# Performance work log

Measured on AMD Instinct MI355X. Metric: run time of the kernel, lower is better.

Reference implementation:

```python
import jax, jax.numpy as jnp
import numpy as np


def _maxpool2x2(t):
    # t: [B, C, H, W] -> [B, C, H//2, W//2]
    B, C, H, W = t.shape
    return t.reshape(B, C, H // 2, 2, W // 2, 2).max(axis=(3, 5))


def setup_inputs() -> dict:
    key = jax.random.key(0)
    k_x, k_t, k_p, k_g, k_o = jax.random.split(key, 5)
    B, C, H, W = 16, 256, 64, 64
    C8, C2 = C // 8, C // 2
    scale = 1.0 / np.sqrt(C)
    return {
        "x": jax.random.normal(k_x, (B, C, H, W), dtype=jnp.float32),
        "w_theta": jax.random.normal(k_t, (C8, C), dtype=jnp.float32) * scale,
        "w_phi": jax.random.normal(k_p, (C8, C), dtype=jnp.float32) * scale,
        "w_g": jax.random.normal(k_g, (C2, C), dtype=jnp.float32) * scale,
        "w_o": jax.random.normal(k_o, (C, C2), dtype=jnp.float32) * (1.0 / np.sqrt(C2)),
        "gamma": jnp.ones((), dtype=jnp.float32),
    }


def reference(x, w_theta, w_phi, w_g, w_o, gamma):
    B, C, H, W = x.shape
    C8, C2 = C // 8, C // 2
    HW = H * W
    # 1x1 conv projections (pure channel GEMMs)
    theta = jnp.einsum("oc,bchw->bohw", w_theta, x)            # [B, C8, H, W]
    phi = _maxpool2x2(jnp.einsum("oc,bchw->bohw", w_phi, x))   # [B, C8, H/2, W/2]
    g = _maxpool2x2(jnp.einsum("oc,bchw->bohw", w_g, x))       # [B, C2, H/2, W/2]
    theta = theta.reshape(B, C8, HW)            # [B, C8, HW]
    phi = phi.reshape(B, C8, HW // 4)           # [B, C8, HW/4]
    g = g.reshape(B, C2, HW // 4)               # [B, C2, HW/4]
    # attention: no scaling, single head (BigGAN style)
    scores = jnp.einsum("bct,bcp->btp", theta, phi)   # [B, HW, HW/4]
    beta = jax.nn.softmax(scores, axis=-1)
    attn = jnp.einsum("bcp,btp->bct", g, beta)        # [B, C2, HW]
    attn = attn.reshape(B, C2, H, W)
    o = jnp.einsum("oc,bchw->bohw", w_o, attn)        # [B, C, H, W]
    return gamma * o + x
```

## Files before the change

### kernel.cpp

```cpp
#include <hip/hip_runtime.h>
#include <stdint.h>


#define B_  16
#define C_  256
#define HW_ 4096
#define C8_ 32
#define C2_ 128
#define P_  1024

#define WS_THETA 0u
#define WS_PHI   2097152u
#define WS_G     2621440u
#define WS_WOG   4718592u
#define WS_BETA  6815744u

__device__ inline unsigned short f2bf(float f) {
    unsigned int u = __builtin_bit_cast(unsigned int, f);
    u = (u + 0x7fffu + ((u >> 16) & 1u)) >> 16;
    return (unsigned short)u;
}
__device__ inline void beta_store4(unsigned short* p, float a, float b, float c, float d) {
    ushort4 v; v.x = f2bf(a); v.y = f2bf(b); v.z = f2bf(c); v.w = f2bf(d);
    *(ushort4*)p = v;
}
__device__ inline void splitbf(float f, unsigned short& h, unsigned short& l) {
    unsigned u = __builtin_bit_cast(unsigned, f);
    h = (unsigned short)(u >> 16);
    float lof = f - __builtin_bit_cast(float, u & 0xffff0000u);
    l = (unsigned short)(__builtin_bit_cast(unsigned, lof) >> 16);
}

typedef __attribute__((ext_vector_type(8))) short bf16x8;
typedef __attribute__((ext_vector_type(8))) unsigned short u16x8;
typedef __attribute__((ext_vector_type(4))) float f32x4;

#define GLOAD_LDS(gsrc, ldst) __builtin_amdgcn_global_load_lds( \
    (__attribute__((address_space(1))) void*)(uintptr_t)(const void*)(gsrc), \
    (__attribute__((address_space(3))) void*)(ldst), 16, 0, 0)

__global__ __launch_bounds__(256, 3) void k1_proj(
    const float* __restrict__ x, const float* __restrict__ w_theta,
    const float* __restrict__ w_phi, const float* __restrict__ w_g,
    float* __restrict__ thetaT_o, float* __restrict__ phiT_o, float* __restrict__ g_o)
{
    const int ht = blockIdx.x, ogrp = blockIdx.y, b = blockIdx.z;
    const int tid = threadIdx.x;
    const int lane = tid & 63, wv = tid >> 6;
    const int lr = lane & 15, lk = lane >> 4;

    __shared__ float xs[64 * 128];
    __shared__ unsigned short WHs[64 * 72];
    __shared__ unsigned short WLs[64 * 72];

    const float* xb = x + ((size_t)b * C_) * HW_ + (size_t)ht * 128;
    const int c_ld = tid >> 2;
    const int sseg = (tid & 3) * 32;
    const int o_ld = tid >> 2;
    const int cseg = (tid & 3) * 16;

    const float* wsrc;
    if (ogrp == 0) wsrc = (o_ld < 32) ? (w_theta + o_ld * 256)
                                      : (w_phi + (o_ld - 32) * 256);
    else if (ogrp == 1) wsrc = w_g + o_ld * 256;
    else wsrc = w_g + (o_ld + 64) * 256;

    f32x4 acc[4][2] = {};

    for (int kc = 0; kc < 4; ++kc) {
        const int c0 = kc * 64;
        __syncthreads();
        {
            const float* src = xb + (size_t)(c0 + c_ld) * HW_ + sseg;
            #pragma unroll
            for (int u = 0; u < 8; ++u)
                *(float4*)&xs[c_ld * 128 + sseg + u * 4] = *(const float4*)&src[u * 4];
        }
        {
            #pragma unroll
            for (int h = 0; h < 2; ++h) {
                u16x8 hi, lo;
                #pragma unroll
                for (int e = 0; e < 8; ++e) {
                    unsigned short hh, ll;
                    splitbf(wsrc[c0 + cseg + h * 8 + e], hh, ll);
                    hi[e] = hh; lo[e] = ll;
                }
                *(u16x8*)&WHs[o_ld * 72 + cseg + h * 8] = hi;
                *(u16x8*)&WLs[o_ld * 72 + cseg + h * 8] = lo;
            }
        }
        __syncthreads();

        #pragma unroll
        for (int ks = 0; ks < 2; ++ks) {
            bf16x8 Ah[4], Al[4];
            #pragma unroll
            for (int mf = 0; mf < 4; ++mf) {
                Ah[mf] = *(const bf16x8*)&WHs[(mf * 16 + lr) * 72 + ks * 32 + lk * 8];
                Al[mf] = *(const bf16x8*)&WLs[(mf * 16 + lr) * 72 + ks * 32 + lk * 8];
            }
            #pragma unroll
            for (int nf = 0; nf < 2; ++nf) {
                const int s = wv * 32 + nf * 16 + lr;
                u16x8 hi, lo;
                #pragma unroll
                for (int e = 0; e < 8; ++e) {
                    unsigned short hh, ll;
                    splitbf(xs[(ks * 32 + lk * 8 + e) * 128 + s], hh, ll);
                    hi[e] = hh; lo[e] = ll;
                }
                const bf16x8 Bh = __builtin_bit_cast(bf16x8, hi);
                const bf16x8 Bl = __builtin_bit_cast(bf16x8, lo);
                #pragma unroll
                for (int mf = 0; mf < 4; ++mf) {
                    acc[mf][nf] = __builtin_amdgcn_mfma_f32_16x16x32_bf16(
                        Ah[mf], Bh, acc[mf][nf], 0, 0, 0);
                    acc[mf][nf] = __builtin_amdgcn_mfma_f32_16x16x32_bf16(
                        Ah[mf], Bl, acc[mf][nf], 0, 0, 0);
                    acc[mf][nf] = __builtin_amdgcn_mfma_f32_16x16x32_bf16(
                        Al[mf], Bh, acc[mf][nf], 0, 0, 0);
                }
            }
        }
    }

    __syncthreads();
    #pragma unroll
    for (int mf = 0; mf < 4; ++mf)
        #pragma unroll
        for (int nf = 0; nf < 2; ++nf)
            #pragma unroll
            for (int r = 0; r < 4; ++r)
                xs[(mf * 16 + lk * 4 + r) * 128 + wv * 32 + nf * 16 + lr]
                    = acc[mf][nf][r];
    __syncthreads();

    if (ogrp == 0) {
        {
            const int s = tid >> 1, o16 = (tid & 1) * 16;
            float* dst = thetaT_o + ((size_t)b * HW_ + (size_t)ht * 128 + s) * 32 + o16;
            #pragma unroll
            for (int u = 0; u < 4; ++u) {
                float4 v;
                v.x = xs[(o16 + u * 4 + 0) * 128 + s];
                v.y = xs[(o16 + u * 4 + 1) * 128 + s];
                v.z = xs[(o16 + u * 4 + 2) * 128 + s];
                v.w = xs[(o16 + u * 4 + 3) * 128 + s];
                *(float4*)&dst[u * 4] = v;
            }
        }
        {
            const int o2 = tid >> 3, wq = (tid & 7) * 4;
            #pragma unroll
            for (int u = 0; u < 4; ++u) {
                int w2 = wq + u;
                float pv = fmaxf(fmaxf(xs[(32 + o2) * 128 + 2 * w2],
                                       xs[(32 + o2) * 128 + 2 * w2 + 1]),
                                 fmaxf(xs[(32 + o2) * 128 + 64 + 2 * w2],
                                       xs[(32 + o2) * 128 + 64 + 2 * w2 + 1]));
                phiT_o[((size_t)b * P_ + (size_t)ht * 32 + w2) * 32 + o2] = pv;
            }
        }
    } else {
        const int base = (ogrp - 1) * 64;
        const int o = tid >> 2, wq = (tid & 3) * 8;
        float* dst = g_o + ((size_t)b * C2_ + base + o) * P_ + (size_t)ht * 32 + wq;
        #pragma unroll
        for (int u = 0; u < 8; ++u) {
            int w2 = wq + u;
            dst[u] = fmaxf(fmaxf(xs[o * 128 + 2 * w2], xs[o * 128 + 2 * w2 + 1]),
                           fmaxf(xs[o * 128 + 64 + 2 * w2], xs[o * 128 + 64 + 2 * w2 + 1]));
        }
    }
}

__global__ __launch_bounds__(256) void k2_wog(
    const float* __restrict__ w_o, const float* __restrict__ g,
    unsigned short* __restrict__ wog)
{
    const int p0 = blockIdx.x * 64, cb = blockIdx.y, b = blockIdx.z;
    const int tid = threadIdx.x, wv = tid >> 6, lane = tid & 63;
    __shared__ float wls[64][128];
    __shared__ float gls[128][64];

    {
        const int o = tid >> 2, q = (tid & 3) * 32;
        const float* src = w_o + (size_t)(cb * 64 + o) * 128 + q;
        #pragma unroll
        for (int u = 0; u < 8; ++u)
            *(float4*)&wls[o][q + u * 4] = *(const float4*)&src[u * 4];
        const int c2 = tid >> 1, h = (tid & 1) * 32;
        const float* gsrc = g + ((size_t)b * C2_ + c2) * P_ + p0 + h;
        #pragma unroll
        for (int u = 0; u < 8; ++u)
            *(float4*)&gls[c2][h + u * 4] = *(const float4*)&gsrc[u * 4];
    }
    __syncthreads();

    float acc[16] = {};
    for (int k4 = 0; k4 < 32; ++k4) {
        float gk[4];
        #pragma unroll
        for (int kk = 0; kk < 4; ++kk) gk[kk] = gls[k4 * 4 + kk][lane];
        #pragma unroll
        for (int i = 0; i < 16; ++i) {
            float4 w4 = *(const float4*)&wls[wv * 16 + i][k4 * 4];
            acc[i] += w4.x * gk[0] + w4.y * gk[1] + w4.z * gk[2] + w4.w * gk[3];
        }
    }
    #pragma unroll
    for (int i = 0; i < 16; ++i)
        wog[((size_t)b * C_ + cb * 64 + wv * 16 + i) * P_ + p0 + lane] = f2bf(acc[i]);
}

__global__ __launch_bounds__(256, 3) void k3_mfma(
    const float* __restrict__ thetaT, const float* __restrict__ phiT,
    unsigned short* __restrict__ beta)
{
    const int t0 = blockIdx.x * 16, b = blockIdx.y;
    const int tid = threadIdx.x, wv = tid >> 6, lane = tid & 63;
    const int lr = lane & 15, lk = lane >> 4;

    __shared__ __align__(16) char sm[44032];
    unsigned short* phH = (unsigned short*)sm;
    unsigned short* phL = (unsigned short*)(sm + 20480);
    unsigned short* thH = (unsigned short*)(sm + 40960);
    unsigned short* thL = (unsigned short*)(sm + 42240);
    float* red = (float*)(sm + 43520);

    if (tid < 128) {
        const int t = tid >> 3, c4 = (tid & 7) * 4;
        float4 v = *(const float4*)&thetaT[((size_t)b * HW_ + t0 + t) * 32 + c4];
        ushort4 hv, lv;
        splitbf(v.x, hv.x, lv.x); splitbf(v.y, hv.y, lv.y);
        splitbf(v.z, hv.z, lv.z); splitbf(v.w, hv.w, lv.w);
        *(ushort4*)&thH[t * 40 + c4] = hv;
        *(ushort4*)&thL[t * 40 + c4] = lv;
    }

    f32x4 sc[16];

    #pragma unroll
    for (int ch = 0; ch < 4; ++ch) {
        __syncthreads();
        {
            const float* src = &phiT[((size_t)b * P_ + ch * 256 + tid) * 32];
            #pragma unroll
            for (int g2 = 0; g2 < 4; ++g2) {
                float4 a = *(const float4*)&src[g2 * 8];
                float4 b4 = *(const float4*)&src[g2 * 8 + 4];
                u16x8 hi, lo;
                unsigned short hh, ll;
                splitbf(a.x, hh, ll);  hi[0] = hh; lo[0] = ll;
                splitbf(a.y, hh, ll);  hi[1] = hh; lo[1] = ll;
                splitbf(a.z, hh, ll);  hi[2] = hh; lo[2] = ll;
                splitbf(a.w, hh, ll);  hi[3] = hh; lo[3] = ll;
                splitbf(b4.x, hh, ll); hi[4] = hh; lo[4] = ll;
                splitbf(b4.y, hh, ll); hi[5] = hh; lo[5] = ll;
                splitbf(b4.z, hh, ll); hi[6] = hh; lo[6] = ll;
                splitbf(b4.w, hh, ll); hi[7] = hh; lo[7] = ll;
                *(u16x8*)&phH[tid * 40 + g2 * 8] = hi;
                *(u16x8*)&phL[tid * 40 + g2 * 8] = lo;
            }
        }
        __syncthreads();

        const bf16x8 Ah = *(const bf16x8*)&thH[lr * 40 + lk * 8];
        const bf16x8 Al = *(const bf16x8*)&thL[lr * 40 + lk * 8];
        #pragma unroll
        for (int q = 0; q < 4; ++q) {
            const int prow = wv * 64 + q * 16 + lr;
            const bf16x8 Bh = *(const bf16x8*)&phH[prow * 40 + lk * 8];
            const bf16x8 Bl = *(const bf16x8*)&phL[prow * 40 + lk * 8];
            f32x4 a = {};
            a = __builtin_amdgcn_mfma_f32_16x16x32_bf16(Ah, Bh, a, 0, 0, 0);
            a = __builtin_amdgcn_mfma_f32_16x16x32_bf16(Ah, Bl, a, 0, 0, 0);
            a = __builtin_amdgcn_mfma_f32_16x16x32_bf16(Al, Bh, a, 0, 0, 0);
            sc[ch * 4 + q] = a;
        }
    }

    float mrow[4], rl[4];
    #pragma unroll
    for (int r = 0; r < 4; ++r) {
        float m = sc[0][r];
        #pragma unroll
        for (int qg = 1; qg < 16; ++qg) m = fmaxf(m, sc[qg][r]);
        #pragma unroll
        for (int off = 1; off < 16; off <<= 1) m = fmaxf(m, __shfl_xor(m, off));
        mrow[r] = m;
    }
    __syncthreads();
    if (lr == 0) {
        #pragma unroll
        for (int r = 0; r < 4; ++r) red[(lk * 4 + r) * 4 + wv] = mrow[r];
    }
    __syncthreads();
    #pragma unroll
    for (int r = 0; r < 4; ++r) {
        const int t = lk * 4 + r;
        mrow[r] = fmaxf(fmaxf(red[t * 4 + 0], red[t * 4 + 1]),
                        fmaxf(red[t * 4 + 2], red[t * 4 + 3]));
    }
    __syncthreads();

    float ssum[4];
    #pragma unroll
    for (int r = 0; r < 4; ++r) {
        float s = 0.f;
        #pragma unroll
        for (int qg = 0; qg < 16; ++qg) {
            float e = __expf(sc[qg][r] - mrow[r]);
            sc[qg][r] = e; s += e;
        }
        #pragma unroll
        for (int off = 1; off < 16; off <<= 1) s += __shfl_xor(s, off);
        ssum[r] = s;
    }
    if (lr == 0) {
        #pragma unroll
        for (int r = 0; r < 4; ++r) red[(lk * 4 + r) * 4 + wv] = ssum[r];
    }
    __syncthreads();
    #pragma unroll
    for (int r = 0; r < 4; ++r) {
        const int t = lk * 4 + r;
        rl[r] = 1.0f / (red[t * 4 + 0] + red[t * 4 + 1] +
                        red[t * 4 + 2] + red[t * 4 + 3]);
    }

    unsigned short* bb = beta + ((size_t)b * HW_ + t0) * P_;
    #pragma unroll
    for (int qg = 0; qg < 16; ++qg) {
        const int p = (qg >> 2) * 256 + wv * 64 + (qg & 3) * 16 + lr;
        #pragma unroll
        for (int r = 0; r < 4; ++r)
            bb[(size_t)(lk * 4 + r) * P_ + p] = f2bf(sc[qg][r] * rl[r]);
    }
}

__global__ __launch_bounds__(256) void k4_mfma(
    const unsigned short* __restrict__ wog, const unsigned short* __restrict__ beta,
    const float* __restrict__ x, const float* __restrict__ gamma_p,
    float* __restrict__ out)
{
    const int t0 = blockIdx.x * 128, c0 = blockIdx.y * 128, b = blockIdx.z;
    const int tid = threadIdx.x, wv = tid >> 6, lane = tid & 63;
    const int wm = wv >> 1, wn = wv & 1;
    const int lr = lane & 15, lk = lane >> 4;
    __shared__ unsigned short As[128 * 64];
    __shared__ unsigned short Bs[128 * 64];

    f32x4 acc[4][4] = {};
    const unsigned short* wog_b  = wog  + ((size_t)b * C_  + c0) * P_;
    const unsigned short* beta_b = beta + ((size_t)b * HW_ + t0) * P_;

    for (int p0 = 0; p0 < 1024; p0 += 64) {
        __syncthreads();
        #pragma unroll
        for (int ch = 0; ch < 4; ++ch) {
            const int i16 = ch * 256 + tid;
            const int row = i16 >> 3, cb8 = i16 & 7;
            GLOAD_LDS(wog_b  + (size_t)row * P_ + p0 + cb8 * 8, &As[i16 * 8]);
            GLOAD_LDS(beta_b + (size_t)row * P_ + p0 + cb8 * 8, &Bs[i16 * 8]);
        }
        __syncthreads();

        #pragma unroll
        for (int ks = 0; ks < 2; ++ks) {
            bf16x8 af[4], bfr[4];
            #pragma unroll
            for (int mf = 0; mf < 4; ++mf)
                af[mf] = *(const bf16x8*)&As[(wm * 64 + mf * 16 + lr) * 64 + ks * 32 + lk * 8];
            #pragma unroll
            for (int nf = 0; nf < 4; ++nf)
                bfr[nf] = *(const bf16x8*)&Bs[(wn * 64 + nf * 16 + lr) * 64 + ks * 32 + lk * 8];
            #pragma unroll
            for (int mf = 0; mf < 4; ++mf)
                #pragma unroll
                for (int nf = 0; nf < 4; ++nf)
                    acc[mf][nf] = __builtin_amdgcn_mfma_f32_16x16x32_bf16(
                        af[mf], bfr[nf], acc[mf][nf], 0, 0, 0);
        }
    }

    const float gm = gamma_p[0];
    #pragma unroll
    for (int mf = 0; mf < 4; ++mf) {
        #pragma unroll
        for (int r = 0; r < 4; ++r) {
            const int co = c0 + wm * 64 + mf * 16 + lk * 4 + r;
            const size_t rowoff = ((size_t)b * C_ + co) * HW_;
            #pragma unroll
            for (int nf = 0; nf < 4; ++nf) {
                const int t = t0 + wn * 64 + nf * 16 + lr;
                out[rowoff + t] = gm * acc[mf][nf][r] + x[rowoff + t];
            }
        }
    }
}

extern "C" void kernel_launch(void* const* d_in, const int* in_sizes, int n_in,
                              void* d_out, int out_size, void* d_ws, size_t ws_size,
                              hipStream_t stream)
{
    const float* x       = (const float*)d_in[0];
    const float* w_theta = (const float*)d_in[1];
    const float* w_phi   = (const float*)d_in[2];
    const float* w_g     = (const float*)d_in[3];
    const float* w_o     = (const float*)d_in[4];
    const float* gamma   = (const float*)d_in[5];
    float* out = (float*)d_out;
    float* ws  = (float*)d_ws;

    float* thetaT         = ws + WS_THETA;
    float* phiT           = ws + WS_PHI;
    float* g              = ws + WS_G;
    unsigned short* wog   = (unsigned short*)(ws + WS_WOG);
    unsigned short* beta  = (unsigned short*)(ws + WS_BETA);

    k1_proj<<<dim3(32, 3, 16), 256, 0, stream>>>(x, w_theta, w_phi, w_g,
                                                 thetaT, phiT, g);
    k2_wog<<<dim3(16, 4, 16), 256, 0, stream>>>(w_o, g, wog);
    k3_mfma<<<dim3(256, 16), 256, 0, stream>>>(thetaT, phiT, beta);
    k4_mfma<<<dim3(32, 2, 16), 256, 0, stream>>>(wog, beta, x, gamma, out);
}
```

Measured before the change: 321.0 us.

## Presplit theta/phi to bf16 hi/lo in projection and enlarge score tiles

The projection kernel now writes theta and phi already split into bf16 high/low halves, so the score kernel no longer converts fp32 per block. The score kernel loads those halves directly into LDS with global_load_lds using an XOR swizzle, and processes 32 query rows per block instead of 16. This halves the number of phi reloads and conversions. k4's LDS tiles also get an XOR swizzle to reduce bank conflicts. In exchange, the score kernel holds twice as many accumulator registers and its occupancy hint drops from 3 to 2.

```diff
diff --git a/kernel.cpp b/kernel.cpp
--- a/kernel.cpp
+++ b/kernel.cpp
@@ -9,20 +9,18 @@
 #define C2_ 128
 #define P_  1024
 
-#define WS_THETA 0u
-#define WS_PHI   2097152u
-#define WS_G     2621440u
-#define WS_WOG   4718592u
-#define WS_BETA  6815744u
+#define WS_THH  0u
+#define WS_THL  1048576u
+#define WS_PHH  2097152u
+#define WS_PHL  2359296u
+#define WS_G    2621440u
+#define WS_WOG  4718592u
+#define WS_BETA 6815744u
 
 __device__ inline unsigned short f2bf(float f) {
     unsigned int u = __builtin_bit_cast(unsigned int, f);
     u = (u + 0x7fffu + ((u >> 16) & 1u)) >> 16;
     return (unsigned short)u;
-}
-__device__ inline void beta_store4(unsigned short* p, float a, float b, float c, float d) {
-    ushort4 v; v.x = f2bf(a); v.y = f2bf(b); v.z = f2bf(c); v.w = f2bf(d);
-    *(ushort4*)p = v;
 }
 __device__ inline void splitbf(float f, unsigned short& h, unsigned short& l) {
     unsigned u = __builtin_bit_cast(unsigned, f);
@@ -42,7 +40,9 @@
 __global__ __launch_bounds__(256, 3) void k1_proj(
     const float* __restrict__ x, const float* __restrict__ w_theta,
     const float* __restrict__ w_phi, const float* __restrict__ w_g,
-    float* __restrict__ thetaT_o, float* __restrict__ phiT_o, float* __restrict__ g_o)
+    unsigned short* __restrict__ thetaTH, unsigned short* __restrict__ thetaTL,
+    unsigned short* __restrict__ phiTH, unsigned short* __restrict__ phiTL,
+    float* __restrict__ g_o)
 {
     const int ht = blockIdx.x, ogrp = blockIdx.y, b = blockIdx.z;
     const int tid = threadIdx.x;
@@ -139,16 +139,18 @@
     if (ogrp == 0) {
         {
             const int s = tid >> 1, o16 = (tid & 1) * 16;
-            float* dst = thetaT_o + ((size_t)b * HW_ + (size_t)ht * 128 + s) * 32 + o16;
-            #pragma unroll
-            for (int u = 0; u < 4; ++u) {
-                float4 v;
-                v.x = xs[(o16 + u * 4 + 0) * 128 + s];
-                v.y = xs[(o16 + u * 4 + 1) * 128 + s];
-                v.z = xs[(o16 + u * 4 + 2) * 128 + s];
-                v.w = xs[(o16 + u * 4 + 3) * 128 + s];
-                *(float4*)&dst[u * 4] = v;
-            }
+            u16x8 h0, h1, l0, l1;
+            #pragma unroll
+            for (int i = 0; i < 8; ++i) {
+                unsigned short hh, ll;
+                splitbf(xs[(o16 + i) * 128 + s], hh, ll);
+                h0[i] = hh; l0[i] = ll;
+                splitbf(xs[(o16 + 8 + i) * 128 + s], hh, ll);
+                h1[i] = hh; l1[i] = ll;
+            }
+            const size_t roff = ((size_t)b * HW_ + (size_t)ht * 128 + s) * 32 + o16;
+            *(u16x8*)&thetaTH[roff] = h0; *(u16x8*)&thetaTH[roff + 8] = h1;
+            *(u16x8*)&thetaTL[roff] = l0; *(u16x8*)&thetaTL[roff + 8] = l1;
         }
         {
             const int o2 = tid >> 3, wq = (tid & 7) * 4;
@@ -159,7 +161,10 @@
                                        xs[(32 + o2) * 128 + 2 * w2 + 1]),
                                  fmaxf(xs[(32 + o2) * 128 + 64 + 2 * w2],
                                        xs[(32 + o2) * 128 + 64 + 2 * w2 + 1]));
-                phiT_o[((size_t)b * P_ + (size_t)ht * 32 + w2) * 32 + o2] = pv;
+                unsigned short hh, ll;
+                splitbf(pv, hh, ll);
+                const size_t poff = ((size_t)b * P_ + (size_t)ht * 32 + w2) * 32 + o2;
+                phiTH[poff] = hh; phiTL[poff] = ll;
             }
         }
     } else {
@@ -214,130 +219,139 @@
         wog[((size_t)b * C_ + cb * 64 + wv * 16 + i) * P_ + p0 + lane] = f2bf(acc[i]);
 }
 
-__global__ __launch_bounds__(256, 3) void k3_mfma(
-    const float* __restrict__ thetaT, const float* __restrict__ phiT,
+__global__ __launch_bounds__(256, 2) void k3_mfma(
+    const unsigned short* __restrict__ thH_g, const unsigned short* __restrict__ thL_g,
+    const unsigned short* __restrict__ phH_g, const unsigned short* __restrict__ phL_g,
     unsigned short* __restrict__ beta)
 {
-    const int t0 = blockIdx.x * 16, b = blockIdx.y;
+    const int t0 = blockIdx.x * 32, b = blockIdx.y;
     const int tid = threadIdx.x, wv = tid >> 6, lane = tid & 63;
     const int lr = lane & 15, lk = lane >> 4;
 
-    __shared__ __align__(16) char sm[44032];
-    unsigned short* phH = (unsigned short*)sm;
-    unsigned short* phL = (unsigned short*)(sm + 20480);
-    unsigned short* thH = (unsigned short*)(sm + 40960);
-    unsigned short* thL = (unsigned short*)(sm + 42240);
-    float* red = (float*)(sm + 43520);
-
-    if (tid < 128) {
-        const int t = tid >> 3, c4 = (tid & 7) * 4;
-        float4 v = *(const float4*)&thetaT[((size_t)b * HW_ + t0 + t) * 32 + c4];
-        ushort4 hv, lv;
-        splitbf(v.x, hv.x, lv.x); splitbf(v.y, hv.y, lv.y);
-        splitbf(v.z, hv.z, lv.z); splitbf(v.w, hv.w, lv.w);
-        *(ushort4*)&thH[t * 40 + c4] = hv;
-        *(ushort4*)&thL[t * 40 + c4] = lv;
-    }
-
-    f32x4 sc[16];
+    __shared__ unsigned short thH[32 * 32], thL[32 * 32];
+    __shared__ unsigned short phH[256 * 32], phL[256 * 32];
+    __shared__ float red[32 * 4];
+
+    {
+        const int u = lane + (wv & 1) * 64;
+        const int row = u >> 2, j = u & 3;
+        const int gj = j ^ ((row >> 1) & 3);
+        const size_t goff = ((size_t)b * HW_ + t0 + row) * 32 + gj * 8;
+        if (wv < 2) GLOAD_LDS(thH_g + goff, &thH[u * 8]);
+        else        GLOAD_LDS(thL_g + goff, &thL[u * 8]);
+    }
+
+    f32x4 sc[2][16] = {};
 
     #pragma unroll
     for (int ch = 0; ch < 4; ++ch) {
         __syncthreads();
-        {
-            const float* src = &phiT[((size_t)b * P_ + ch * 256 + tid) * 32];
-            #pragma unroll
-            for (int g2 = 0; g2 < 4; ++g2) {
-                float4 a = *(const float4*)&src[g2 * 8];
-                float4 b4 = *(const float4*)&src[g2 * 8 + 4];
-                u16x8 hi, lo;
-                unsigned short hh, ll;
-                splitbf(a.x, hh, ll);  hi[0] = hh; lo[0] = ll;
-                splitbf(a.y, hh, ll);  hi[1] = hh; lo[1] = ll;
-                splitbf(a.z, hh, ll);  hi[2] = hh; lo[2] = ll;
-                splitbf(a.w, hh, ll);  hi[3] = hh; lo[3] = ll;
-                splitbf(b4.x, hh, ll); hi[4] = hh; lo[4] = ll;
-                splitbf(b4.y, hh, ll); hi[5] = hh; lo[5] = ll;
-                splitbf(b4.z, hh, ll); hi[6] = hh; lo[6] = ll;
-                splitbf(b4.w, hh, ll); hi[7] = hh; lo[7] = ll;
-                *(u16x8*)&phH[tid * 40 + g2 * 8] = hi;
-                *(u16x8*)&phL[tid * 40 + g2 * 8] = lo;
-            }
-        }
-        __syncthreads();
-
-        const bf16x8 Ah = *(const bf16x8*)&thH[lr * 40 + lk * 8];
-        const bf16x8 Al = *(const bf16x8*)&thL[lr * 40 + lk * 8];
+        #pragma unroll
+        for (int it = 0; it < 4; ++it) {
+            const int u = it * 256 + tid;
+            const int row = u >> 2, j = u & 3;
+            const int gj = j ^ ((row >> 1) & 3);
+            const size_t goff = ((size_t)b * P_ + ch * 256 + row) * 32 + gj * 8;
+            GLOAD_LDS(phH_g + goff, &phH[u * 8]);
+            GLOAD_LDS(phL_g + goff, &phL[u * 8]);
+        }
+        __syncthreads();
+
+        bf16x8 Ah[2], Al[2];
+        #pragma unroll
+        for (int mf = 0; mf < 2; ++mf) {
+            const int tr = mf * 16 + lr;
+            const int ja = lk ^ ((tr >> 1) & 3);
+            Ah[mf] = *(const bf16x8*)&thH[tr * 32 + ja * 8];
+            Al[mf] = *(const bf16x8*)&thL[tr * 32 + ja * 8];
+        }
         #pragma unroll
         for (int q = 0; q < 4; ++q) {
-            const int prow = wv * 64 + q * 16 + lr;
-            const bf16x8 Bh = *(const bf16x8*)&phH[prow * 40 + lk * 8];
-            const bf16x8 Bl = *(const bf16x8*)&phL[prow * 40 + lk * 8];
-            f32x4 a = {};
-            a = __builtin_amdgcn_mfma_f32_16x16x32_bf16(Ah, Bh, a, 0, 0, 0);
-            a = __builtin_amdgcn_mfma_f32_16x16x32_bf16(Ah, Bl, a, 0, 0, 0);
-            a = __builtin_amdgcn_mfma_f32_16x16x32_bf16(Al, Bh, a, 0, 0, 0);
-            sc[ch * 4 + q] = a;
-        }
-    }
-
-    float mrow[4], rl[4];
-    #pragma unroll
-    for (int r = 0; r < 4; ++r) {
-        float m = sc[0][r];
-        #pragma unroll
-        for (int qg = 1; qg < 16; ++qg) m = fmaxf(m, sc[qg][r]);
-        #pragma unroll
-        for (int off = 1; off < 16; off <<= 1) m = fmaxf(m, __shfl_xor(m, off));
-        mrow[r] = m;
-    }
-    __syncthreads();
-    if (lr == 0) {
-        #pragma unroll
-        for (int r = 0; r < 4; ++r) red[(lk * 4 + r) * 4 + wv] = mrow[r];
-    }
-    __syncthreads();
-    #pragma unroll
-    for (int r = 0; r < 4; ++r) {
-        const int t = lk * 4 + r;
-        mrow[r] = fmaxf(fmaxf(red[t * 4 + 0], red[t * 4 + 1]),
-                        fmaxf(red[t * 4 + 2], red[t * 4 + 3]));
-    }
-    __syncthreads();
-
-    float ssum[4];
-    #pragma unroll
-    for (int r = 0; r < 4; ++r) {
-        float s = 0.f;
+            const int pr = wv * 64 + q * 16 + lr;
+            const int jb = lk ^ ((pr >> 1) & 3);
+            const bf16x8 Bh = *(const bf16x8*)&phH[pr * 32 + jb * 8];
+            const bf16x8 Bl = *(const bf16x8*)&phL[pr * 32 + jb * 8];
+            #pragma unroll
+            for (int mf = 0; mf < 2; ++mf) {
+                f32x4 a = sc[mf][ch * 4 + q];
+                a = __builtin_amdgcn_mfma_f32_16x16x32_bf16(Ah[mf], Bh, a, 0, 0, 0);
+                a = __builtin_amdgcn_mfma_f32_16x16x32_bf16(Ah[mf], Bl, a, 0, 0, 0);
+                a = __builtin_amdgcn_mfma_f32_16x16x32_bf16(Al[mf], Bh, a, 0, 0, 0);
+                sc[mf][ch * 4 + q] = a;
+            }
+        }
+    }
+
+    float mrow[2][4];
+    #pragma unroll
+    for (int mf = 0; mf < 2; ++mf)
+        #pragma unroll
+        for (int r = 0; r < 4; ++r) {
+            float m = sc[mf][0][r];
+            #pragma unroll
+            for (int qg = 1; qg < 16; ++qg) m = fmaxf(m, sc[mf][qg][r]);
+            #pragma unroll
+            for (int off = 1; off < 16; off <<= 1) m = fmaxf(m, __shfl_xor(m, off));
+            mrow[mf][r] = m;
+        }
+    if (lr == 0)
+        #pragma unroll
+        for (int mf = 0; mf < 2; ++mf)
+            #pragma unroll
+            for (int r = 0; r < 4; ++r)
+                red[(mf * 16 + lk * 4 + r) * 4 + wv] = mrow[mf][r];
+    __syncthreads();
+    #pragma unroll
+    for (int mf = 0; mf < 2; ++mf)
+        #pragma unroll
+        for (int r = 0; r < 4; ++r) {
+            const int t = mf * 16 + lk * 4 + r;
+            mrow[mf][r] = fmaxf(fmaxf(red[t * 4 + 0], red[t * 4 + 1]),
+                                fmaxf(red[t * 4 + 2], red[t * 4 + 3]));
+        }
+    __syncthreads();
+
+    float rl[2][4];
+    #pragma unroll
+    for (int mf = 0; mf < 2; ++mf)
+        #pragma unroll
+        for (int r = 0; r < 4; ++r) {
+            float s = 0.f;
+            #pragma unroll
+            for (int qg = 0; qg < 16; ++qg) {
+                float e = __expf(sc[mf][qg][r] - mrow[mf][r]);
+                sc[mf][qg][r] = e; s += e;
+            }
+            #pragma unroll
+            for (int off = 1; off < 16; off <<= 1) s += __shfl_xor(s, off);
+            rl[mf][r] = s;
+        }
+    if (lr == 0)
+        #pragma unroll
+        for (int mf = 0; mf < 2; ++mf)
+            #pragma unroll
+            for (int r = 0; r < 4; ++r)
+                red[(mf * 16 + lk * 4 + r) * 4 + wv] = rl[mf][r];
+    __syncthreads();
+    #pragma unroll
+    for (int mf = 0; mf < 2; ++mf)
+        #pragma unroll
+        for (int r = 0; r < 4; ++r) {
+            const int t = mf * 16 + lk * 4 + r;
+            rl[mf][r] = 1.0f / (red[t * 4 + 0] + red[t * 4 + 1] +
+                                red[t * 4 + 2] + red[t * 4 + 3]);
+        }
+
+    unsigned short* bb = beta + ((size_t)b * HW_ + t0) * P_;
+    #pragma unroll
+    for (int mf = 0; mf < 2; ++mf)
         #pragma unroll
         for (int qg = 0; qg < 16; ++qg) {
-            float e = __expf(sc[qg][r] - mrow[r]);
-            sc[qg][r] = e; s += e;
-        }
-        #pragma unroll
-        for (int off = 1; off < 16; off <<= 1) s += __shfl_xor(s, off);
-        ssum[r] = s;
-    }
-    if (lr == 0) {
-        #pragma unroll
-        for (int r = 0; r < 4; ++r) red[(lk * 4 + r) * 4 + wv] = ssum[r];
-    }
-    __syncthreads();
-    #pragma unroll
-    for (int r = 0; r < 4; ++r) {
-        const int t = lk * 4 + r;
-        rl[r] = 1.0f / (red[t * 4 + 0] + red[t * 4 + 1] +
-                        red[t * 4 + 2] + red[t * 4 + 3]);
-    }
-
-    unsigned short* bb = beta + ((size_t)b * HW_ + t0) * P_;
-    #pragma unroll
-    for (int qg = 0; qg < 16; ++qg) {
-        const int p = (qg >> 2) * 256 + wv * 64 + (qg & 3) * 16 + lr;
-        #pragma unroll
-        for (int r = 0; r < 4; ++r)
-            bb[(size_t)(lk * 4 + r) * P_ + p] = f2bf(sc[qg][r] * rl[r]);
-    }
+            const int p = (qg >> 2) * 256 + wv * 64 + (qg & 3) * 16 + lr;
+            #pragma unroll
+            for (int r = 0; r < 4; ++r)
+                bb[(size_t)(mf * 16 + lk * 4 + r) * P_ + p] = f2bf(sc[mf][qg][r] * rl[mf][r]);
+        }
 }
 
 __global__ __launch_bounds__(256) void k4_mfma(
@@ -362,8 +376,9 @@
         for (int ch = 0; ch < 4; ++ch) {
             const int i16 = ch * 256 + tid;
             const int row = i16 >> 3, cb8 = i16 & 7;
-            GLOAD_LDS(wog_b  + (size_t)row * P_ + p0 + cb8 * 8, &As[i16 * 8]);
-            GLOAD_LDS(beta_b + (size_t)row * P_ + p0 + cb8 * 8, &Bs[i16 * 8]);
+            const int gcb = cb8 ^ (row & 7);
+            GLOAD_LDS(wog_b  + (size_t)row * P_ + p0 + gcb * 8, &As[i16 * 8]);
+            GLOAD_LDS(beta_b + (size_t)row * P_ + p0 + gcb * 8, &Bs[i16 * 8]);
         }
         __syncthreads();
 
@@ -371,11 +386,17 @@
         for (int ks = 0; ks < 2; ++ks) {
             bf16x8 af[4], bfr[4];
             #pragma unroll
-            for (int mf = 0; mf < 4; ++mf)
-                af[mf] = *(const bf16x8*)&As[(wm * 64 + mf * 16 + lr) * 64 + ks * 32 + lk * 8];
-            #pragma unroll
-            for (int nf = 0; nf < 4; ++nf)
-                bfr[nf] = *(const bf16x8*)&Bs[(wn * 64 + nf * 16 + lr) * 64 + ks * 32 + lk * 8];
+            for (int mf = 0; mf < 4; ++mf) {
+                const int arow = wm * 64 + mf * 16 + lr;
+                const int ja = (ks * 4 + lk) ^ (arow & 7);
+                af[mf] = *(const bf16x8*)&As[arow * 64 + ja * 8];
+            }
+            #pragma unroll
+            for (int nf = 0; nf < 4; ++nf) {
+                const int brow = wn * 64 + nf * 16 + lr;
+                const int jb = (ks * 4 + lk) ^ (brow & 7);
+                bfr[nf] = *(const bf16x8*)&Bs[brow * 64 + jb * 8];
+            }
             #pragma unroll
             for (int mf = 0; mf < 4; ++mf)
                 #pragma unroll
@@ -414,15 +435,17 @@
     float* out = (float*)d_out;
     float* ws  = (float*)d_ws;
 
-    float* thetaT         = ws + WS_THETA;
-    float* phiT           = ws + WS_PHI;
-    float* g              = ws + WS_G;
-    unsigned short* wog   = (unsigned short*)(ws + WS_WOG);
-    unsigned short* beta  = (unsigned short*)(ws + WS_BETA);
+    unsigned short* thH  = (unsigned short*)(ws + WS_THH);
+    unsigned short* thL  = (unsigned short*)(ws + WS_THL);
+    unsigned short* phH  = (unsigned short*)(ws + WS_PHH);
+    unsigned short* phL  = (unsigned short*)(ws + WS_PHL);
+    float* g             = ws + WS_G;
+    unsigned short* wog  = (unsigned short*)(ws + WS_WOG);
+    unsigned short* beta = (unsigned short*)(ws + WS_BETA);
 
     k1_proj<<<dim3(32, 3, 16), 256, 0, stream>>>(x, w_theta, w_phi, w_g,
-                                                 thetaT, phiT, g);
+                                                 thH, thL, phH, phL, g);
     k2_wog<<<dim3(16, 4, 16), 256, 0, stream>>>(w_o, g, wog);
-    k3_mfma<<<dim3(256, 16), 256, 0, stream>>>(thetaT, phiT, beta);
+    k3_mfma<<<dim3(128, 16), 256, 0, stream>>>(thH, thL, phH, phL, beta);
     k4_mfma<<<dim3(32, 2, 16), 256, 0, stream>>>(wog, beta, x, gamma, out);
 }
```

Measured after the change: 288.3 us. 1.11x faster.
